# Optimization experiments

Hardware: AMD Instinct MI355X
Metric: run time of the kernel (lower is better)

The kernel has to match this reference:

```python
import jax, jax.numpy as jnp
import numpy as np

N_HEADS, N_LEVELS, N_POINTS = 8, 4, 4


def _bilinear(im, grid, H, W):
    # im: [N, D, H*W] flattened level feature, grid: [N, Q, P, 2] in [-1, 1]
    # F.grid_sample bilinear, padding_mode='zeros', align_corners=False
    N, Q, P, _ = grid.shape
    D = im.shape[1]
    gx = ((grid[..., 0] + 1.0) * W - 1.0) * 0.5
    gy = ((grid[..., 1] + 1.0) * H - 1.0) * 0.5
    x0f = jnp.floor(gx)
    y0f = jnp.floor(gy)
    x0 = x0f.astype(jnp.int32)
    y0 = y0f.astype(jnp.int32)
    wx1 = gx - x0f
    wy1 = gy - y0f
    acc = jnp.zeros((N, D, Q * P), im.dtype)
    corners = ((0, 0, (1 - wx1) * (1 - wy1)), (1, 0, wx1 * (1 - wy1)),
               (0, 1, (1 - wx1) * wy1), (1, 1, wx1 * wy1))
    for dx, dy, wgt in corners:
        xi = x0 + dx
        yi = y0 + dy
        valid = (xi >= 0) & (xi < W) & (yi >= 0) & (yi < H)
        idx = jnp.clip(yi, 0, H - 1) * W + jnp.clip(xi, 0, W - 1)
        v = jnp.take_along_axis(im, idx.reshape(N, 1, Q * P), axis=2)  # [N,D,QP]
        acc = acc + v * jnp.where(valid, wgt, 0.0).reshape(N, 1, Q * P)
    return acc.reshape(N, D, Q, P)


def _forward(query, value, reference_points, shapes_np,
             w_off, b_off, w_attn, b_attn, w_val, b_val, w_out, b_out):
    B, Q, E = query.shape
    H_, L, P = N_HEADS, N_LEVELS, N_POINTS
    D = E // H_
    v = (value @ w_val + b_val).reshape(B, -1, H_, D)  # [B, Nv, H, D]
    off = (query @ w_off + b_off).reshape(B, Q, H_, L, P, 2)
    attn = (query @ w_attn + b_attn).reshape(B, Q, H_, L * P)
    attn = jax.nn.softmax(attn, axis=-1).reshape(B, Q, H_, L, P)
    # offset_scale = [W_l, H_l] per level
    scale = jnp.asarray(np.stack([shapes_np[:, 1], shapes_np[:, 0]], -1), jnp.float32)
    locs = reference_points[:, :, None, :, None, :] + off / scale[None, None, None, :, None, :]
    grid = 2.0 * locs - 1.0  # [B, Q, H, L, P, 2]
    starts = np.concatenate([[0], np.cumsum(shapes_np[:, 0] * shapes_np[:, 1])]).astype(int)
    out = jnp.zeros((B * H_, D, Q), query.dtype)
    for lvl in range(L):
        h, w = int(shapes_np[lvl, 0]), int(shapes_np[lvl, 1])
        feat = v[:, starts[lvl]:starts[lvl + 1]]                      # [B, h*w, H, D]
        feat = feat.transpose(0, 2, 3, 1).reshape(B * H_, D, h * w)   # [BH, D, hw]
        g = jnp.transpose(grid[:, :, :, lvl], (0, 2, 1, 3, 4)).reshape(B * H_, Q, P, 2)
        sampled = _bilinear(feat, g, h, w)                            # [BH, D, Q, P]
        wl = jnp.transpose(attn[:, :, :, lvl], (0, 2, 1, 3)).reshape(B * H_, 1, Q, P)
        out = out + (sampled * wl).sum(-1)                            # [BH, D, Q]
    out = out.reshape(B, H_ * D, Q).transpose(0, 2, 1)                # [B, Q, E]
    return out @ w_out + b_out


def setup_inputs() -> dict:
    key = jax.random.key(0)
    ks = jax.random.split(key, 12)
    B, Q, E = 2, 19947, 256
    L, H_, P = N_LEVELS, N_HEADS, N_POINTS
    shapes = jnp.array([[100, 150], [50, 75], [25, 38], [13, 19]], dtype=jnp.int64)
    s = 0.02
    return {
        'query': jax.random.normal(ks[0], (B, Q, E), jnp.float32),
        'value': jax.random.normal(ks[1], (B, Q, E), jnp.float32),
        'reference_points': jax.random.uniform(ks[2], (B, Q, L, 2), jnp.float32),
        'spatial_shapes': shapes,
        'w_off': jax.random.normal(ks[3], (E, H_ * L * P * 2), jnp.float32) * s,
        'b_off': jax.random.normal(ks[4], (H_ * L * P * 2,), jnp.float32) * s,
        'w_attn': jax.random.normal(ks[5], (E, H_ * L * P), jnp.float32) * s,
        'b_attn': jax.random.normal(ks[6], (H_ * L * P,), jnp.float32) * s,
        'w_val': jax.random.normal(ks[7], (E, E), jnp.float32) * s,
        'b_val': jax.random.normal(ks[8], (E,), jnp.float32) * s,
        'w_out': jax.random.normal(ks[9], (E, E), jnp.float32) * s,
        'b_out': jax.random.normal(ks[10], (E,), jnp.float32) * s,
    }


def reference(query, value, reference_points, spatial_shapes,
              w_off, b_off, w_attn, b_attn, w_val, b_val, w_out, b_out):
    shapes_np = np.asarray(spatial_shapes)
    return _forward(query, value, reference_points, shapes_np,
                    w_off, b_off, w_attn, b_attn, w_val, b_val, w_out, b_out)
```

## Files before the change

kernel.cpp:

```cpp
#include <hip/hip_runtime.h>
#include <math.h>
#include <type_traits>

#define B_    2
#define Q_    19947
#define E_    256
#define H_    8
#define D_    32
#define L_    4
#define P_    4

typedef __bf16 bf16_t;
typedef bf16_t bf16x8 __attribute__((ext_vector_type(8)));
typedef bf16_t bf16x4 __attribute__((ext_vector_type(4)));
typedef float  f32x4  __attribute__((ext_vector_type(4)));

__global__ __launch_bounds__(256)
void transpose_all(const float* __restrict__ w_val, const float* __restrict__ w_off,
                   const float* __restrict__ w_attn, const float* __restrict__ w_out,
                   bf16_t* __restrict__ WtV, bf16_t* __restrict__ WtQ,
                   bf16_t* __restrict__ WtO)
{
    const float* in; bf16_t* out; int N;
    switch (blockIdx.z) {
        case 0:  in = w_val;  out = WtV;             N = 256; break;
        case 1:  in = w_off;  out = WtQ;             N = 256; break;
        case 2:  in = w_attn; out = WtQ + 256 * 256; N = 128; break;
        default: in = w_out;  out = WtO;             N = 256; break;
    }
    const int nt = blockIdx.x * 32;
    if (nt >= N) return;
    const int kt = blockIdx.y * 32;

    __shared__ float tile[32][33];
    const int x  = threadIdx.x & 31;
    const int y0 = threadIdx.x >> 5;
    #pragma unroll
    for (int p = 0; p < 4; ++p)
        tile[y0 + p * 8][x] = in[(size_t)(kt + y0 + p * 8) * N + nt + x];
    __syncthreads();
    #pragma unroll
    for (int p = 0; p < 4; ++p)
        out[(size_t)(nt + y0 + p * 8) * 256 + kt + x] = (bf16_t)tile[x][y0 + p * 8];
}

template<bool FUSED>
__global__ __launch_bounds__(256, 5)
void gemm_mfma(const float* __restrict__ Aval, const float* __restrict__ Aqry,
               const bf16_t* __restrict__ Aout,
               const bf16_t* __restrict__ WtV, const bf16_t* __restrict__ WtQ,
               const bf16_t* __restrict__ WtO,
               const float* __restrict__ b_val, const float* __restrict__ b_off,
               const float* __restrict__ b_attn, const float* __restrict__ b_out,
               bf16_t* __restrict__ v_proj, float* __restrict__ off_b,
               float* __restrict__ attn_b, float* __restrict__ outp, int M)
{
    constexpr int K = 256, BK = 32, NIT = K / BK;
    __shared__ __align__(16) bf16_t As[2][64][40];
    __shared__ __align__(16) bf16_t Bs[2][128][40];

    const int t    = threadIdx.x;
    const int m0   = blockIdx.x * 64;
    const int by   = blockIdx.y;
    const bool isVal = FUSED && (by < 2);
    const float*  Af = isVal ? Aval : Aqry;
    const bf16_t* Wt = FUSED ? (isVal ? WtV : WtQ) : WtO;
    const int n0     = FUSED ? (isVal ? by * 128 : (by - 2) * 128) : by * 128;

    const int lane = t & 63;
    const int w    = t >> 6;
    const int wm   = w & 1, wn = w >> 1;
    const int quad = lane >> 4, l16 = lane & 15;

    const int srow = t >> 2;
    const int skc  = (t & 3) * 8;

    f32x4 acc[2][4];
    #pragma unroll
    for (int i = 0; i < 2; ++i)
        #pragma unroll
        for (int j = 0; j < 4; ++j) {
            f32x4 z = {0.f, 0.f, 0.f, 0.f};
            acc[i][j] = z;
        }

    bf16x8 aval;
    uint4  bval0, bval1;

    auto load_stage = [&](int k0) {
        const int gm = m0 + srow;
        if constexpr (FUSED) {
            if (gm < M) {
                const float4 v0 = *(const float4*)(Af + (size_t)gm * 256 + k0 + skc);
                const float4 v1 = *(const float4*)(Af + (size_t)gm * 256 + k0 + skc + 4);
                aval[0] = (bf16_t)v0.x; aval[1] = (bf16_t)v0.y;
                aval[2] = (bf16_t)v0.z; aval[3] = (bf16_t)v0.w;
                aval[4] = (bf16_t)v1.x; aval[5] = (bf16_t)v1.y;
                aval[6] = (bf16_t)v1.z; aval[7] = (bf16_t)v1.w;
            } else {
                #pragma unroll
                for (int i = 0; i < 8; ++i) aval[i] = (bf16_t)0.f;
            }
        } else {
            if (gm < M) {
                aval = *(const bf16x8*)(Aout + (size_t)gm * 256 + k0 + skc);
            } else {
                #pragma unroll
                for (int i = 0; i < 8; ++i) aval[i] = (bf16_t)0.f;
            }
        }
        bval0 = *(const uint4*)(Wt + (size_t)(n0 + srow)      * 256 + k0 + skc);
        bval1 = *(const uint4*)(Wt + (size_t)(n0 + srow + 64) * 256 + k0 + skc);
    };
    auto store_stage = [&](int buf) {
        *(bf16x8*)&As[buf][srow][skc]    = aval;
        *(uint4*)&Bs[buf][srow][skc]     = bval0;
        *(uint4*)&Bs[buf][srow + 64][skc] = bval1;
    };

    load_stage(0);
    store_stage(0);
    int cur = 0;

    #pragma unroll
    for (int it = 0; it < NIT; ++it) {
        __syncthreads();
        if (it + 1 < NIT)
            load_stage((it + 1) * BK);

        bf16x8 af[2], bfr[4];
        #pragma unroll
        for (int i = 0; i < 2; ++i)
            af[i] = *(const bf16x8*)&As[cur][wm * 32 + i * 16 + l16][quad * 8];
        #pragma unroll
        for (int j = 0; j < 4; ++j)
            bfr[j] = *(const bf16x8*)&Bs[cur][wn * 64 + j * 16 + l16][quad * 8];
        #pragma unroll
        for (int i = 0; i < 2; ++i)
            #pragma unroll
            for (int j = 0; j < 4; ++j)
                acc[i][j] = __builtin_amdgcn_mfma_f32_16x16x32_bf16(af[i], bfr[j], acc[i][j], 0, 0, 0);

        if (it + 1 < NIT)
            store_stage(cur ^ 1);
        cur ^= 1;
    }

    #pragma unroll
    for (int j = 0; j < 4; ++j) {
        const int gn = n0 + wn * 64 + j * 16 + l16;
        float bv;
        if constexpr (FUSED)
            bv = isVal ? b_val[gn] : (gn < 256 ? b_off[gn] : b_attn[gn - 256]);
        else
            bv = b_out[gn];
        #pragma unroll
        for (int i = 0; i < 2; ++i) {
            #pragma unroll
            for (int r = 0; r < 4; ++r) {
                const int gm = m0 + wm * 32 + i * 16 + quad * 4 + r;
                if (gm < M) {
                    const float val = acc[i][j][r] + bv;
                    if constexpr (FUSED) {
                        if (isVal)
                            v_proj[(size_t)gm * 256 + gn] = (bf16_t)val;
                        else if (gn < 256)
                            off_b[(size_t)gm * 256 + gn] = val;
                        else
                            attn_b[(size_t)gm * 128 + (gn - 256)] = val;
                    } else {
                        outp[(size_t)gm * 256 + gn] = val;
                    }
                }
            }
        }
    }
}

__global__ __launch_bounds__(256)
void msda_sample_kernel(const bf16_t* __restrict__ v,
                        const float* __restrict__ off,
                        const float* __restrict__ attn,
                        const float* __restrict__ ref,
                        bf16_t* __restrict__ out_tmp,
                        int BQH)
{
    constexpr int SH[4] = {100, 50, 25, 13};
    constexpr int SW[4] = {150, 75, 38, 19};
    constexpr int ST[4] = {0, 15000, 18750, 19700};

    const int g    = blockIdx.x * 64 + (threadIdx.x >> 2);
    const int lane = threadIdx.x & 3;
    if (g >= BQH) return;

    const int h  = g & (H_ - 1);
    const int bq = g >> 3;
    const int b  = bq / Q_;

    const bf16_t* vbase = v + ((size_t)b * Q_) * E_ + h * D_ + lane * 8;
    const float* offp   = off  + (size_t)bq * 256 + h * 32;
    const float* attnp  = attn + (size_t)bq * 128 + h * 16;

    float aw[16];
    #pragma unroll
    for (int i = 0; i < 4; ++i) {
        const float4 x = *(const float4*)(attnp + i * 4);
        aw[i * 4 + 0] = x.x; aw[i * 4 + 1] = x.y; aw[i * 4 + 2] = x.z; aw[i * 4 + 3] = x.w;
    }
    float mx = aw[0];
    #pragma unroll
    for (int i = 1; i < 16; ++i) mx = fmaxf(mx, aw[i]);
    float sum = 0.f;
    #pragma unroll
    for (int i = 0; i < 16; ++i) { aw[i] = expf(aw[i] - mx); sum += aw[i]; }
    const float inv = 1.f / sum;
    #pragma unroll
    for (int i = 0; i < 16; ++i) aw[i] *= inv;

    const float4 r01 = *(const float4*)(ref + (size_t)bq * 8);
    const float4 r23 = *(const float4*)(ref + (size_t)bq * 8 + 4);
    const float rx[4] = {r01.x, r01.z, r23.x, r23.z};
    const float ry[4] = {r01.y, r01.w, r23.y, r23.w};

    float acc[8] = {0.f, 0.f, 0.f, 0.f, 0.f, 0.f, 0.f, 0.f};

    #pragma unroll
    for (int l = 0; l < L_; ++l) {
        const float fW = (float)SW[l], fH = (float)SH[l];
        const int   Ww = SW[l], Hh = SH[l], st = ST[l];
        #pragma unroll
        for (int pp = 0; pp < 2; ++pp) {
            const float4 o2 = *(const float4*)(offp + l * 8 + pp * 4);
            #pragma unroll
            for (int q = 0; q < 2; ++q) {
                const int   p  = pp * 2 + q;
                const float ox = q ? o2.z : o2.x;
                const float oy = q ? o2.w : o2.y;
                const float wA = aw[l * 4 + p];
                const float gx = fmaf(rx[l], fW, ox) - 0.5f;
                const float gy = fmaf(ry[l], fH, oy) - 0.5f;
                const float x0f = floorf(gx), y0f = floorf(gy);
                const int   x0  = (int)x0f,   y0  = (int)y0f;
                const float wx1 = gx - x0f,   wy1 = gy - y0f;
                const float wx0 = 1.f - wx1,  wy0 = 1.f - wy1;

                const float mxw0 = ((unsigned)x0     < (unsigned)Ww) ? wx0 : 0.f;
                const float mxw1 = ((unsigned)(x0+1) < (unsigned)Ww) ? wx1 : 0.f;
                const float myw0 = ((unsigned)y0     < (unsigned)Hh) ? wy0 : 0.f;
                const float myw1 = ((unsigned)(y0+1) < (unsigned)Hh) ? wy1 : 0.f;
                const int xc0 = min(max(x0, 0),     Ww - 1);
                const int xc1 = min(max(x0 + 1, 0), Ww - 1);
                const int yc0 = min(max(y0, 0),     Hh - 1);
                const int yc1 = min(max(y0 + 1, 0), Hh - 1);

                const float w00 = wA * mxw0 * myw0;
                const float w10 = wA * mxw1 * myw0;
                const float w01 = wA * mxw0 * myw1;
                const float w11 = wA * mxw1 * myw1;

                const bf16x8 s00 = *(const bf16x8*)(vbase + (size_t)(st + yc0 * Ww + xc0) * E_);
                const bf16x8 s10 = *(const bf16x8*)(vbase + (size_t)(st + yc0 * Ww + xc1) * E_);
                const bf16x8 s01 = *(const bf16x8*)(vbase + (size_t)(st + yc1 * Ww + xc0) * E_);
                const bf16x8 s11 = *(const bf16x8*)(vbase + (size_t)(st + yc1 * Ww + xc1) * E_);

                #pragma unroll
                for (int c = 0; c < 8; ++c) {
                    acc[c] = fmaf(w00, (float)s00[c], acc[c]);
                    acc[c] = fmaf(w10, (float)s10[c], acc[c]);
                    acc[c] = fmaf(w01, (float)s01[c], acc[c]);
                    acc[c] = fmaf(w11, (float)s11[c], acc[c]);
                }
            }
        }
    }

    bf16x8 o;
    #pragma unroll
    for (int c = 0; c < 8; ++c) o[c] = (bf16_t)acc[c];
    *(bf16x8*)(out_tmp + (size_t)bq * E_ + h * D_ + lane * 8) = o;
}

extern "C" void kernel_launch(void* const* d_in, const int* in_sizes, int n_in,
                              void* d_out, int out_size, void* d_ws, size_t ws_size,
                              hipStream_t stream)
{
    const float* query  = (const float*)d_in[0];
    const float* value  = (const float*)d_in[1];
    const float* refpts = (const float*)d_in[2];
    const float* w_off  = (const float*)d_in[4];
    const float* b_off  = (const float*)d_in[5];
    const float* w_attn = (const float*)d_in[6];
    const float* b_attn = (const float*)d_in[7];
    const float* w_val  = (const float*)d_in[8];
    const float* b_val  = (const float*)d_in[9];
    const float* w_out  = (const float*)d_in[10];
    const float* b_out  = (const float*)d_in[11];
    float* out = (float*)d_out;

    const int BQ = B_ * Q_;

    char* ws = (char*)d_ws;
    bf16_t* v_proj  = (bf16_t*)ws;                    ws += (size_t)BQ * 256 * 2;
    float*  off_b   = (float*)ws;                     ws += (size_t)BQ * 256 * 4;
    float*  attn_b  = (float*)ws;                     ws += (size_t)BQ * 128 * 4;
    bf16_t* out_tmp = (bf16_t*)ws;                    ws += (size_t)BQ * 256 * 2;
    bf16_t* WtV     = (bf16_t*)ws;                    ws += (size_t)256 * 256 * 2;
    bf16_t* WtQ     = (bf16_t*)ws;                    ws += (size_t)384 * 256 * 2;
    bf16_t* WtO     = (bf16_t*)ws;

    const dim3 blk(256);

    transpose_all<<<dim3(8, 8, 4), blk, 0, stream>>>(w_val, w_off, w_attn, w_out,
                                                     WtV, WtQ, WtO);

    const int mg = (BQ + 63) / 64;

    gemm_mfma<true><<<dim3(mg, 5), blk, 0, stream>>>(
        value, query, (const bf16_t*)nullptr, WtV, WtQ, WtO,
        b_val, b_off, b_attn, b_out, v_proj, off_b, attn_b, out, BQ);

    const int BQH = BQ * H_;
    msda_sample_kernel<<<(BQH + 63) / 64, blk, 0, stream>>>(
        v_proj, off_b, attn_b, refpts, out_tmp, BQH);

    gemm_mfma<false><<<dim3(mg, 2), blk, 0, stream>>>(
        (const float*)nullptr, (const float*)nullptr, out_tmp, WtV, WtQ, WtO,
        b_val, b_off, b_attn, b_out, v_proj, off_b, attn_b, out, BQ);
}
```

Measured before the change: 305.6 us.

## Fuse output projection GEMM into sampling kernel and switch to fp16

Merges the deformable-attention sampling kernel with the output projection: each block samples 16 queries across all heads into shared memory, then runs MFMA against the transposed output weight and writes the final result. This removes the intermediate out_tmp round trip through global memory and one kernel launch. All bf16 storage and MFMA calls also switch to fp16, which changes precision and range behaviour. The trade-off is that every block re-reads the full 256x256 output weight from global/L2, and with only 16 rows per block the MFMA work is less efficient than a tiled GEMM.

```diff
diff --git a/kernel.cpp b/kernel.cpp
--- a/kernel.cpp
+++ b/kernel.cpp
@@ -1,6 +1,5 @@
 #include <hip/hip_runtime.h>
 #include <math.h>
-#include <type_traits>
 
 #define B_    2
 #define Q_    19947
@@ -10,18 +9,18 @@
 #define L_    4
 #define P_    4
 
-typedef __bf16 bf16_t;
-typedef bf16_t bf16x8 __attribute__((ext_vector_type(8)));
-typedef bf16_t bf16x4 __attribute__((ext_vector_type(4)));
-typedef float  f32x4  __attribute__((ext_vector_type(4)));
+typedef _Float16 f16_t;
+typedef f16_t f16x8 __attribute__((ext_vector_type(8)));
+typedef f16_t f16x4 __attribute__((ext_vector_type(4)));
+typedef float f32x4 __attribute__((ext_vector_type(4)));
 
 __global__ __launch_bounds__(256)
 void transpose_all(const float* __restrict__ w_val, const float* __restrict__ w_off,
                    const float* __restrict__ w_attn, const float* __restrict__ w_out,
-                   bf16_t* __restrict__ WtV, bf16_t* __restrict__ WtQ,
-                   bf16_t* __restrict__ WtO)
+                   f16_t* __restrict__ WtV, f16_t* __restrict__ WtQ,
+                   f16_t* __restrict__ WtO)
 {
-    const float* in; bf16_t* out; int N;
+    const float* in; f16_t* out; int N;
     switch (blockIdx.z) {
         case 0:  in = w_val;  out = WtV;             N = 256; break;
         case 1:  in = w_off;  out = WtQ;             N = 256; break;
@@ -41,31 +40,28 @@
     __syncthreads();
     #pragma unroll
     for (int p = 0; p < 4; ++p)
-        out[(size_t)(nt + y0 + p * 8) * 256 + kt + x] = (bf16_t)tile[x][y0 + p * 8];
+        out[(size_t)(nt + y0 + p * 8) * 256 + kt + x] = (f16_t)tile[x][y0 + p * 8];
 }
 
-template<bool FUSED>
 __global__ __launch_bounds__(256, 5)
-void gemm_mfma(const float* __restrict__ Aval, const float* __restrict__ Aqry,
-               const bf16_t* __restrict__ Aout,
-               const bf16_t* __restrict__ WtV, const bf16_t* __restrict__ WtQ,
-               const bf16_t* __restrict__ WtO,
+void gemm_proj(const float* __restrict__ Aval, const float* __restrict__ Aqry,
+               const f16_t* __restrict__ WtV, const f16_t* __restrict__ WtQ,
                const float* __restrict__ b_val, const float* __restrict__ b_off,
-               const float* __restrict__ b_attn, const float* __restrict__ b_out,
-               bf16_t* __restrict__ v_proj, float* __restrict__ off_b,
-               float* __restrict__ attn_b, float* __restrict__ outp, int M)
+               const float* __restrict__ b_attn,
+               f16_t* __restrict__ v_proj, float* __restrict__ off_b,
+               float* __restrict__ attn_b, int M)
 {
     constexpr int K = 256, BK = 32, NIT = K / BK;
-    __shared__ __align__(16) bf16_t As[2][64][40];
-    __shared__ __align__(16) bf16_t Bs[2][128][40];
+    __shared__ __align__(16) f16_t As[2][64][40];
+    __shared__ __align__(16) f16_t Bs[2][128][40];
 
     const int t    = threadIdx.x;
     const int m0   = blockIdx.x * 64;
     const int by   = blockIdx.y;
-    const bool isVal = FUSED && (by < 2);
+    const bool isVal = (by < 2);
     const float*  Af = isVal ? Aval : Aqry;
-    const bf16_t* Wt = FUSED ? (isVal ? WtV : WtQ) : WtO;
-    const int n0     = FUSED ? (isVal ? by * 128 : (by - 2) * 128) : by * 128;
+    const f16_t*  Wt = isVal ? WtV : WtQ;
+    const int n0     = isVal ? by * 128 : (by - 2) * 128;
 
     const int lane = t & 63;
     const int w    = t >> 6;
@@ -84,37 +80,28 @@
             acc[i][j] = z;
         }
 
-    bf16x8 aval;
-    uint4  bval0, bval1;
+    f16x8 aval;
+    uint4 bval0, bval1;
 
     auto load_stage = [&](int k0) {
         const int gm = m0 + srow;
-        if constexpr (FUSED) {
-            if (gm < M) {
-                const float4 v0 = *(const float4*)(Af + (size_t)gm * 256 + k0 + skc);
-                const float4 v1 = *(const float4*)(Af + (size_t)gm * 256 + k0 + skc + 4);
-                aval[0] = (bf16_t)v0.x; aval[1] = (bf16_t)v0.y;
-                aval[2] = (bf16_t)v0.z; aval[3] = (bf16_t)v0.w;
-                aval[4] = (bf16_t)v1.x; aval[5] = (bf16_t)v1.y;
-                aval[6] = (bf16_t)v1.z; aval[7] = (bf16_t)v1.w;
-            } else {
-                #pragma unroll
-                for (int i = 0; i < 8; ++i) aval[i] = (bf16_t)0.f;
-            }
+        if (gm < M) {
+            const float4 v0 = *(const float4*)(Af + (size_t)gm * 256 + k0 + skc);
+            const float4 v1 = *(const float4*)(Af + (size_t)gm * 256 + k0 + skc + 4);
+            aval[0] = (f16_t)v0.x; aval[1] = (f16_t)v0.y;
+            aval[2] = (f16_t)v0.z; aval[3] = (f16_t)v0.w;
+            aval[4] = (f16_t)v1.x; aval[5] = (f16_t)v1.y;
+            aval[6] = (f16_t)v1.z; aval[7] = (f16_t)v1.w;
         } else {
-            if (gm < M) {
-                aval = *(const bf16x8*)(Aout + (size_t)gm * 256 + k0 + skc);
-            } else {
-                #pragma unroll
-                for (int i = 0; i < 8; ++i) aval[i] = (bf16_t)0.f;
-            }
+            #pragma unroll
+            for (int i = 0; i < 8; ++i) aval[i] = (f16_t)0.f;
         }
         bval0 = *(const uint4*)(Wt + (size_t)(n0 + srow)      * 256 + k0 + skc);
         bval1 = *(const uint4*)(Wt + (size_t)(n0 + srow + 64) * 256 + k0 + skc);
     };
     auto store_stage = [&](int buf) {
-        *(bf16x8*)&As[buf][srow][skc]    = aval;
-        *(uint4*)&Bs[buf][srow][skc]     = bval0;
+        *(f16x8*)&As[buf][srow][skc]      = aval;
+        *(uint4*)&Bs[buf][srow][skc]      = bval0;
         *(uint4*)&Bs[buf][srow + 64][skc] = bval1;
     };
 
@@ -128,18 +115,18 @@
         if (it + 1 < NIT)
             load_stage((it + 1) * BK);
 
-        bf16x8 af[2], bfr[4];
+        f16x8 af[2], bfr[4];
         #pragma unroll
         for (int i = 0; i < 2; ++i)
-            af[i] = *(const bf16x8*)&As[cur][wm * 32 + i * 16 + l16][quad * 8];
+            af[i] = *(const f16x8*)&As[cur][wm * 32 + i * 16 + l16][quad * 8];
         #pragma unroll
         for (int j = 0; j < 4; ++j)
-            bfr[j] = *(const bf16x8*)&Bs[cur][wn * 64 + j * 16 + l16][quad * 8];
+            bfr[j] = *(const f16x8*)&Bs[cur][wn * 64 + j * 16 + l16][quad * 8];
         #pragma unroll
         for (int i = 0; i < 2; ++i)
             #pragma unroll
             for (int j = 0; j < 4; ++j)
-                acc[i][j] = __builtin_amdgcn_mfma_f32_16x16x32_bf16(af[i], bfr[j], acc[i][j], 0, 0, 0);
+                acc[i][j] = __builtin_amdgcn_mfma_f32_16x16x32_f16(af[i], bfr[j], acc[i][j], 0, 0, 0);
 
         if (it + 1 < NIT)
             store_stage(cur ^ 1);
@@ -149,11 +136,7 @@
     #pragma unroll
     for (int j = 0; j < 4; ++j) {
         const int gn = n0 + wn * 64 + j * 16 + l16;
-        float bv;
-        if constexpr (FUSED)
-            bv = isVal ? b_val[gn] : (gn < 256 ? b_off[gn] : b_attn[gn - 256]);
-        else
-            bv = b_out[gn];
+        const float bv = isVal ? b_val[gn] : (gn < 256 ? b_off[gn] : b_attn[gn - 256]);
         #pragma unroll
         for (int i = 0; i < 2; ++i) {
             #pragma unroll
@@ -161,123 +144,171 @@
                 const int gm = m0 + wm * 32 + i * 16 + quad * 4 + r;
                 if (gm < M) {
                     const float val = acc[i][j][r] + bv;
-                    if constexpr (FUSED) {
-                        if (isVal)
-                            v_proj[(size_t)gm * 256 + gn] = (bf16_t)val;
-                        else if (gn < 256)
-                            off_b[(size_t)gm * 256 + gn] = val;
-                        else
-                            attn_b[(size_t)gm * 128 + (gn - 256)] = val;
-                    } else {
-                        outp[(size_t)gm * 256 + gn] = val;
-                    }
+                    if (isVal)
+                        v_proj[(size_t)gm * 256 + gn] = (f16_t)val;
+                    else if (gn < 256)
+                        off_b[(size_t)gm * 256 + gn] = val;
+                    else
+                        attn_b[(size_t)gm * 128 + (gn - 256)] = val;
                 }
             }
         }
     }
 }
 
-__global__ __launch_bounds__(256)
-void msda_sample_kernel(const bf16_t* __restrict__ v,
-                        const float* __restrict__ off,
-                        const float* __restrict__ attn,
-                        const float* __restrict__ ref,
-                        bf16_t* __restrict__ out_tmp,
-                        int BQH)
+__global__ __launch_bounds__(256, 4)
+void msda_fused(const f16_t* __restrict__ v,
+                const float* __restrict__ off,
+                const float* __restrict__ attn,
+                const float* __restrict__ ref,
+                const f16_t* __restrict__ WoT,
+                const float* __restrict__ b_out,
+                float* __restrict__ out,
+                int BQ)
 {
     constexpr int SH[4] = {100, 50, 25, 13};
     constexpr int SW[4] = {150, 75, 38, 19};
     constexpr int ST[4] = {0, 15000, 18750, 19700};
 
-    const int g    = blockIdx.x * 64 + (threadIdx.x >> 2);
-    const int lane = threadIdx.x & 3;
-    if (g >= BQH) return;
-
-    const int h  = g & (H_ - 1);
-    const int bq = g >> 3;
-    const int b  = bq / Q_;
-
-    const bf16_t* vbase = v + ((size_t)b * Q_) * E_ + h * D_ + lane * 8;
-    const float* offp   = off  + (size_t)bq * 256 + h * 32;
-    const float* attnp  = attn + (size_t)bq * 128 + h * 16;
-
-    float aw[16];
-    #pragma unroll
-    for (int i = 0; i < 4; ++i) {
-        const float4 x = *(const float4*)(attnp + i * 4);
-        aw[i * 4 + 0] = x.x; aw[i * 4 + 1] = x.y; aw[i * 4 + 2] = x.z; aw[i * 4 + 3] = x.w;
-    }
-    float mx = aw[0];
-    #pragma unroll
-    for (int i = 1; i < 16; ++i) mx = fmaxf(mx, aw[i]);
-    float sum = 0.f;
-    #pragma unroll
-    for (int i = 0; i < 16; ++i) { aw[i] = expf(aw[i] - mx); sum += aw[i]; }
-    const float inv = 1.f / sum;
-    #pragma unroll
-    for (int i = 0; i < 16; ++i) aw[i] *= inv;
-
-    const float4 r01 = *(const float4*)(ref + (size_t)bq * 8);
-    const float4 r23 = *(const float4*)(ref + (size_t)bq * 8 + 4);
-    const float rx[4] = {r01.x, r01.z, r23.x, r23.z};
-    const float ry[4] = {r01.y, r01.w, r23.y, r23.w};
-
-    float acc[8] = {0.f, 0.f, 0.f, 0.f, 0.f, 0.f, 0.f, 0.f};
-
-    #pragma unroll
-    for (int l = 0; l < L_; ++l) {
-        const float fW = (float)SW[l], fH = (float)SH[l];
-        const int   Ww = SW[l], Hh = SH[l], st = ST[l];
-        #pragma unroll
-        for (int pp = 0; pp < 2; ++pp) {
-            const float4 o2 = *(const float4*)(offp + l * 8 + pp * 4);
-            #pragma unroll
-            for (int q = 0; q < 2; ++q) {
-                const int   p  = pp * 2 + q;
-                const float ox = q ? o2.z : o2.x;
-                const float oy = q ? o2.w : o2.y;
-                const float wA = aw[l * 4 + p];
-                const float gx = fmaf(rx[l], fW, ox) - 0.5f;
-                const float gy = fmaf(ry[l], fH, oy) - 0.5f;
-                const float x0f = floorf(gx), y0f = floorf(gy);
-                const int   x0  = (int)x0f,   y0  = (int)y0f;
-                const float wx1 = gx - x0f,   wy1 = gy - y0f;
-                const float wx0 = 1.f - wx1,  wy0 = 1.f - wy1;
-
-                const float mxw0 = ((unsigned)x0     < (unsigned)Ww) ? wx0 : 0.f;
-                const float mxw1 = ((unsigned)(x0+1) < (unsigned)Ww) ? wx1 : 0.f;
-                const float myw0 = ((unsigned)y0     < (unsigned)Hh) ? wy0 : 0.f;
-                const float myw1 = ((unsigned)(y0+1) < (unsigned)Hh) ? wy1 : 0.f;
-                const int xc0 = min(max(x0, 0),     Ww - 1);
-                const int xc1 = min(max(x0 + 1, 0), Ww - 1);
-                const int yc0 = min(max(y0, 0),     Hh - 1);
-                const int yc1 = min(max(y0 + 1, 0), Hh - 1);
-
-                const float w00 = wA * mxw0 * myw0;
-                const float w10 = wA * mxw1 * myw0;
-                const float w01 = wA * mxw0 * myw1;
-                const float w11 = wA * mxw1 * myw1;
-
-                const bf16x8 s00 = *(const bf16x8*)(vbase + (size_t)(st + yc0 * Ww + xc0) * E_);
-                const bf16x8 s10 = *(const bf16x8*)(vbase + (size_t)(st + yc0 * Ww + xc1) * E_);
-                const bf16x8 s01 = *(const bf16x8*)(vbase + (size_t)(st + yc1 * Ww + xc0) * E_);
-                const bf16x8 s11 = *(const bf16x8*)(vbase + (size_t)(st + yc1 * Ww + xc1) * E_);
-
+    __shared__ __align__(16) f16_t Samp[16][264];
+
+    const int t   = threadIdx.x;
+    const int bq0 = blockIdx.x * 16;
+
+    #pragma unroll
+    for (int r = 0; r < 2; ++r) {
+        const int g    = t >> 2;
+        const int qi   = (g >> 3) + r * 8;
+        const int h    = g & 7;
+        const int lane = t & 3;
+        const int bq   = bq0 + qi;
+
+        float acc[8] = {0.f, 0.f, 0.f, 0.f, 0.f, 0.f, 0.f, 0.f};
+
+        if (bq < BQ) {
+            const int b = bq / Q_;
+            const f16_t* vbase = v + ((size_t)b * Q_) * E_ + h * D_ + lane * 8;
+            const float* offp  = off  + (size_t)bq * 256 + h * 32;
+            const float* attnp = attn + (size_t)bq * 128 + h * 16;
+
+            float aw[16];
+            #pragma unroll
+            for (int i = 0; i < 4; ++i) {
+                const float4 x = *(const float4*)(attnp + i * 4);
+                aw[i*4+0] = x.x; aw[i*4+1] = x.y; aw[i*4+2] = x.z; aw[i*4+3] = x.w;
+            }
+            float mx = aw[0];
+            #pragma unroll
+            for (int i = 1; i < 16; ++i) mx = fmaxf(mx, aw[i]);
+            float sum = 0.f;
+            #pragma unroll
+            for (int i = 0; i < 16; ++i) { aw[i] = expf(aw[i] - mx); sum += aw[i]; }
+            const float inv = 1.f / sum;
+            #pragma unroll
+            for (int i = 0; i < 16; ++i) aw[i] *= inv;
+
+            const float4 r01 = *(const float4*)(ref + (size_t)bq * 8);
+            const float4 r23 = *(const float4*)(ref + (size_t)bq * 8 + 4);
+            const float rx[4] = {r01.x, r01.z, r23.x, r23.z};
+            const float ry[4] = {r01.y, r01.w, r23.y, r23.w};
+
+            #pragma unroll
+            for (int l = 0; l < L_; ++l) {
+                const float fW = (float)SW[l], fH = (float)SH[l];
+                const int   Ww = SW[l], Hh = SH[l], st = ST[l];
                 #pragma unroll
-                for (int c = 0; c < 8; ++c) {
-                    acc[c] = fmaf(w00, (float)s00[c], acc[c]);
-                    acc[c] = fmaf(w10, (float)s10[c], acc[c]);
-                    acc[c] = fmaf(w01, (float)s01[c], acc[c]);
-                    acc[c] = fmaf(w11, (float)s11[c], acc[c]);
+                for (int pp = 0; pp < 2; ++pp) {
+                    const float4 o2 = *(const float4*)(offp + l * 8 + pp * 4);
+                    #pragma unroll
+                    for (int q = 0; q < 2; ++q) {
+                        const int   p  = pp * 2 + q;
+                        const float ox = q ? o2.z : o2.x;
+                        const float oy = q ? o2.w : o2.y;
+                        const float wA = aw[l * 4 + p];
+                        const float gx = fmaf(rx[l], fW, ox) - 0.5f;
+                        const float gy = fmaf(ry[l], fH, oy) - 0.5f;
+                        const float x0f = floorf(gx), y0f = floorf(gy);
+                        const int   x0  = (int)x0f,   y0  = (int)y0f;
+                        const float wx1 = gx - x0f,   wy1 = gy - y0f;
+                        const float wx0 = 1.f - wx1,  wy0 = 1.f - wy1;
+
+                        const float mxw0 = ((unsigned)x0     < (unsigned)Ww) ? wx0 : 0.f;
+                        const float mxw1 = ((unsigned)(x0+1) < (unsigned)Ww) ? wx1 : 0.f;
+                        const float myw0 = ((unsigned)y0     < (unsigned)Hh) ? wy0 : 0.f;
+                        const float myw1 = ((unsigned)(y0+1) < (unsigned)Hh) ? wy1 : 0.f;
+                        const int xc0 = min(max(x0, 0),     Ww - 1);
+                        const int xc1 = min(max(x0 + 1, 0), Ww - 1);
+                        const int yc0 = min(max(y0, 0),     Hh - 1);
+                        const int yc1 = min(max(y0 + 1, 0), Hh - 1);
+
+                        const float w00 = wA * mxw0 * myw0;
+                        const float w10 = wA * mxw1 * myw0;
+                        const float w01 = wA * mxw0 * myw1;
+                        const float w11 = wA * mxw1 * myw1;
+
+                        const f16x8 s00 = *(const f16x8*)(vbase + (size_t)(st + yc0 * Ww + xc0) * E_);
+                        const f16x8 s10 = *(const f16x8*)(vbase + (size_t)(st + yc0 * Ww + xc1) * E_);
+                        const f16x8 s01 = *(const f16x8*)(vbase + (size_t)(st + yc1 * Ww + xc0) * E_);
+                        const f16x8 s11 = *(const f16x8*)(vbase + (size_t)(st + yc1 * Ww + xc1) * E_);
+
+                        #pragma unroll
+                        for (int c = 0; c < 8; ++c) {
+                            acc[c] = fmaf(w00, (float)s00[c], acc[c]);
+                            acc[c] = fmaf(w10, (float)s10[c], acc[c]);
+                            acc[c] = fmaf(w01, (float)s01[c], acc[c]);
+                            acc[c] = fmaf(w11, (float)s11[c], acc[c]);
+                        }
+                    }
                 }
             }
         }
-    }
-
-    bf16x8 o;
-    #pragma unroll
-    for (int c = 0; c < 8; ++c) o[c] = (bf16_t)acc[c];
-    *(bf16x8*)(out_tmp + (size_t)bq * E_ + h * D_ + lane * 8) = o;
+
+        f16x8 o;
+        #pragma unroll
+        for (int c = 0; c < 8; ++c) o[c] = (f16_t)acc[c];
+        *(f16x8*)&Samp[qi][h * 32 + lane * 8] = o;
+    }
+
+    __syncthreads();
+
+    const int lane = t & 63;
+    const int w    = t >> 6;
+    const int quad = lane >> 4, l16 = lane & 15;
+
+    f16x8 af[8];
+    #pragma unroll
+    for (int kf = 0; kf < 8; ++kf)
+        af[kf] = *(const f16x8*)&Samp[l16][kf * 32 + quad * 8];
+
+    f32x4 acc4[4];
+    #pragma unroll
+    for (int j = 0; j < 4; ++j) {
+        f32x4 z = {0.f, 0.f, 0.f, 0.f};
+        acc4[j] = z;
+    }
+
+    #pragma unroll
+    for (int j = 0; j < 4; ++j) {
+        const int n = w * 64 + j * 16 + l16;
+        const f16_t* bp = WoT + (size_t)n * 256 + quad * 8;
+        #pragma unroll
+        for (int kf = 0; kf < 8; ++kf) {
+            const f16x8 bfr = *(const f16x8*)(bp + kf * 32);
+            acc4[j] = __builtin_amdgcn_mfma_f32_16x16x32_f16(af[kf], bfr, acc4[j], 0, 0, 0);
+        }
+    }
+
+    #pragma unroll
+    for (int j = 0; j < 4; ++j) {
+        const int n  = w * 64 + j * 16 + l16;
+        const float bv = b_out[n];
+        #pragma unroll
+        for (int r = 0; r < 4; ++r) {
+            const int gm = bq0 + quad * 4 + r;
+            if (gm < BQ)
+                out[(size_t)gm * 256 + n] = acc4[j][r] + bv;
+        }
+    }
 }
 
 extern "C" void kernel_launch(void* const* d_in, const int* in_sizes, int n_in,
@@ -300,13 +331,12 @@
     const int BQ = B_ * Q_;
 
     char* ws = (char*)d_ws;
-    bf16_t* v_proj  = (bf16_t*)ws;                    ws += (size_t)BQ * 256 * 2;
-    float*  off_b   = (float*)ws;                     ws += (size_t)BQ * 256 * 4;
-    float*  attn_b  = (float*)ws;                     ws += (size_t)BQ * 128 * 4;
-    bf16_t* out_tmp = (bf16_t*)ws;                    ws += (size_t)BQ * 256 * 2;
-    bf16_t* WtV     = (bf16_t*)ws;                    ws += (size_t)256 * 256 * 2;
-    bf16_t* WtQ     = (bf16_t*)ws;                    ws += (size_t)384 * 256 * 2;
-    bf16_t* WtO     = (bf16_t*)ws;
+    f16_t* v_proj = (f16_t*)ws;                       ws += (size_t)BQ * 256 * 2;
+    float* off_b  = (float*)ws;                       ws += (size_t)BQ * 256 * 4;
+    float* attn_b = (float*)ws;                       ws += (size_t)BQ * 128 * 4;
+    f16_t* WtV    = (f16_t*)ws;                       ws += (size_t)256 * 256 * 2;
+    f16_t* WtQ    = (f16_t*)ws;                       ws += (size_t)384 * 256 * 2;
+    f16_t* WtO    = (f16_t*)ws;
 
     const dim3 blk(256);
 
@@ -315,15 +345,10 @@
 
     const int mg = (BQ + 63) / 64;
 
-    gemm_mfma<true><<<dim3(mg, 5), blk, 0, stream>>>(
-        value, query, (const bf16_t*)nullptr, WtV, WtQ, WtO,
-        b_val, b_off, b_attn, b_out, v_proj, off_b, attn_b, out, BQ);
-
-    const int BQH = BQ * H_;
-    msda_sample_kernel<<<(BQH + 63) / 64, blk, 0, stream>>>(
-        v_proj, off_b, attn_b, refpts, out_tmp, BQH);
-
-    gemm_mfma<false><<<dim3(mg, 2), blk, 0, stream>>>(
-        (const float*)nullptr, (const float*)nullptr, out_tmp, WtV, WtQ, WtO,
-        b_val, b_off, b_attn, b_out, v_proj, off_b, attn_b, out, BQ);
+    gemm_proj<<<dim3(mg, 5), blk, 0, stream>>>(
+        value, query, WtV, WtQ, b_val, b_off, b_attn,
+        v_proj, off_b, attn_b, BQ);
+
+    msda_fused<<<dim3((BQ + 15) / 16), blk, 0, stream>>>(
+        v_proj, off_b, attn_b, refpts, WtO, b_out, out, BQ);
 }
```

New measurement: 297.2 us. 2.7% less time.
